# Optimization experiments

Hardware: AMD Instinct MI355X
Metric: run time of the kernel (lower is better)

The kernel has to match this reference:

```python
import jax, jax.numpy as jnp
import numpy as np

B, H, S, Dh = 4, 16, 2048, 64
NEG = -1.0e9


def setup_inputs() -> dict:
    key = jax.random.key(0)
    kq, kk, kv = jax.random.split(key, 3)
    q = jax.random.normal(kq, (B, H, S, Dh), dtype=jnp.float32)
    k = jax.random.normal(kk, (B, H, S, Dh), dtype=jnp.float32)
    v = jax.random.normal(kv, (B, H, S, Dh), dtype=jnp.float32)
    # causal mask: 1.0 where attention is disallowed (j > i), matching mask * -1e9
    mask = jnp.triu(jnp.ones((S, S), dtype=jnp.float32), k=1)[None, None, :, :]
    return {"q": q, "k": k, "v": v, "mask": mask}


def reference(q, k, v, mask):
    # scaled dot-product attention: softmax(QK^T / sqrt(Dh) + mask * -1e9) V
    dim_k = jnp.asarray(k.shape[-1], dtype=jnp.float32)
    logits = jnp.einsum("bhsd,bhtd->bhst", q, k) / jnp.sqrt(dim_k)
    logits = logits + mask * NEG
    weights = jax.nn.softmax(logits, axis=-1)
    return jnp.einsum("bhst,bhtd->bhsd", weights, v)
```

## Files before the change

kernel.cpp:

```cpp
#include <hip/hip_runtime.h>

#define S_LEN 2048
#define DH 64

typedef float f32x4 __attribute__((ext_vector_type(4)));
typedef __bf16 bf16x8 __attribute__((ext_vector_type(8)));

#define PT_STRIDE 36

__device__ __forceinline__ unsigned short f2bf(float f) {
    unsigned u = __builtin_bit_cast(unsigned, f);
    u += 0x7fffu + ((u >> 16) & 1u);
    return (unsigned short)(u >> 16);
}

__device__ __forceinline__ uint4 pack8(const float* s) {
    unsigned short h[8];
#pragma unroll
    for (int i = 0; i < 8; ++i) h[i] = f2bf(s[i]);
    return *(const uint4*)h;
}

__device__ __forceinline__ unsigned pack_rn(float a, float b) {
    unsigned ua = __builtin_bit_cast(unsigned, a) + 0x8000u;
    unsigned ub = __builtin_bit_cast(unsigned, b) + 0x8000u;
    return __builtin_amdgcn_perm(ub, ua, 0x07060302u);
}

__global__ __launch_bounds__(256) void prep_kv(const float* __restrict__ k,
                                               const float* __restrict__ v,
                                               uint4* __restrict__ kimg,
                                               uint4* __restrict__ vimg) {
    __shared__ unsigned short tr[64 * 40];
    const int bid = blockIdx.x;
    const int t = threadIdx.x;
    if (bid < 4096) {
        const int r = t >> 3, b = t & 7;
        const int srcblk = b ^ (r & 7);
        const float* src = k + ((size_t)bid * 32 + r) * 64 + srcblk * 8;
        float buf[8];
        *(float4*)&buf[0] = *(const float4*)src;
        *(float4*)&buf[4] = *(const float4*)(src + 4);
        kimg[(size_t)bid * 256 + t] = pack8(buf);
    } else {
        const int vb = bid - 4096;
        const int r = t >> 3, cb = t & 7;
        const float* src = v + ((size_t)vb * 32 + r) * 64 + cb * 8;
        float buf[8];
        *(float4*)&buf[0] = *(const float4*)src;
        *(float4*)&buf[4] = *(const float4*)(src + 4);
#pragma unroll
        for (int i = 0; i < 8; ++i)
            tr[(cb * 8 + i) * 40 + r] = f2bf(buf[i]);
        __syncthreads();
        const int d = t >> 2, kb = t & 3;
        const int skb = kb ^ ((d >> 1) & 3);
        vimg[(size_t)vb * 256 + t] = *(const uint4*)&tr[d * 40 + skb * 8];
    }
}

template <bool MASKED>
__device__ __forceinline__ void tile_body(
    const unsigned short* __restrict__ kt, const unsigned short* __restrict__ vt,
    unsigned short* __restrict__ pw,
    bf16x8 qf0, bf16x8 qf1, f32x4* acc, float& l_part,
    int jt, int ig, int quad, int c)
{
    f32x4 st[2];
    const int sw = c & 7;
#pragma unroll
    for (int mt = 0; mt < 2; ++mt) {
        const unsigned short* kr = kt + (mt * 16 + c) * 64;
        bf16x8 ka0 = __builtin_bit_cast(bf16x8, *(const uint4*)(kr + ((quad ^ sw) << 3)));
        bf16x8 ka1 = __builtin_bit_cast(bf16x8, *(const uint4*)(kr + (((quad | 4) ^ sw) << 3)));
        f32x4 a = (f32x4){0.f, 0.f, 0.f, 0.f};
        a = __builtin_amdgcn_mfma_f32_16x16x32_bf16(ka0, qf0, a, 0, 0, 0);
        a = __builtin_amdgcn_mfma_f32_16x16x32_bf16(ka1, qf1, a, 0, 0, 0);
        st[mt] = a;
    }

    float p[8];
#pragma unroll
    for (int mt = 0; mt < 2; ++mt)
#pragma unroll
        for (int r = 0; r < 4; ++r) {
            float e = exp2f(st[mt][r]);
            if (MASKED) {
                const int jg = jt * 32 + mt * 16 + quad * 4 + r;
                e = (jg > ig) ? 0.f : e;
            }
            p[mt * 4 + r] = e;
        }
    const float s01 = (p[0] + p[1]) + (p[2] + p[3]);
    const float s23 = (p[4] + p[5]) + (p[6] + p[7]);
    l_part += s01 + s23;

    unsigned* pb = (unsigned*)pw + c * (PT_STRIDE / 2);
#pragma unroll
    for (int mt = 0; mt < 2; ++mt)
#pragma unroll
        for (int rp = 0; rp < 2; ++rp)
            pb[mt * 8 + quad * 2 + rp] = pack_rn(p[mt * 4 + 2 * rp], p[mt * 4 + 2 * rp + 1]);

    const unsigned short* pr = pw + c * PT_STRIDE + quad * 8;
    uint2 lo = *(const uint2*)pr;
    uint2 hi = *(const uint2*)(pr + 4);
    uint4 pu; pu.x = lo.x; pu.y = lo.y; pu.z = hi.x; pu.w = hi.y;
    bf16x8 pf = __builtin_bit_cast(bf16x8, pu);

    const int vsw = (c >> 1) & 3;
#pragma unroll
    for (int dc = 0; dc < 4; ++dc) {
        const unsigned short* vp = vt + (dc * 16 + c) * 32 + ((quad ^ vsw) << 3);
        bf16x8 vf = __builtin_bit_cast(bf16x8, *(const uint4*)vp);
        acc[dc] = __builtin_amdgcn_mfma_f32_16x16x32_bf16(pf, vf, acc[dc], 0, 0, 0);
    }
}

__global__ __launch_bounds__(256) void fa_kernel(
    const float* __restrict__ q,
    const uint4* __restrict__ kimg,
    const uint4* __restrict__ vimg,
    float* __restrict__ out)
{
    __shared__ unsigned short kt[32 * 64];
    __shared__ unsigned short vt[64 * 32];
    __shared__ unsigned short pt[4][16 * PT_STRIDE];

    const int tid  = threadIdx.x;
    const int lane = tid & 63;
    const int wave = tid >> 6;
    const int quad = lane >> 4;
    const int c    = lane & 15;

    const int bid  = blockIdx.x;
    const int bh   = bid & 63;
    const int qblk = 31 - (bid >> 6);

    const int qtile   = qblk * 4 + wave;
    const int qbase   = qtile * 16;
    const int diag    = qtile >> 1;
    const int jt_last = 2 * qblk + 1;

    const size_t head_off = (size_t)bh * S_LEN * DH;

    const float SCALE = 0.125f * 1.4426950408889634f;
    const float* qrow = q + head_off + (size_t)(qbase + c) * DH;
    float qtmp[8];
#pragma unroll
    for (int i = 0; i < 8; ++i) qtmp[i] = qrow[quad * 8 + i] * SCALE;
    bf16x8 qf0 = __builtin_bit_cast(bf16x8, pack8(qtmp));
#pragma unroll
    for (int i = 0; i < 8; ++i) qtmp[i] = qrow[32 + quad * 8 + i] * SCALE;
    bf16x8 qf1 = __builtin_bit_cast(bf16x8, pack8(qtmp));

    f32x4 acc[4];
#pragma unroll
    for (int dc = 0; dc < 4; ++dc) acc[dc] = (f32x4){0.f, 0.f, 0.f, 0.f};
    float l_part = 0.f;
    const int ig = qbase + c;

    const uint4* kin = kimg + (size_t)bh * 64 * 256 + tid;
    const uint4* vin = vimg + (size_t)bh * 64 * 256 + tid;
    unsigned short* pw = pt[wave];

    uint4 kreg = kin[0];
    uint4 vreg = vin[0];
    for (int jt = 0; jt <= jt_last; ++jt) {
        __syncthreads();
        ((uint4*)kt)[tid] = kreg;
        ((uint4*)vt)[tid] = vreg;
        if (jt < jt_last) {
            kreg = kin[(jt + 1) * 256];
            vreg = vin[(jt + 1) * 256];
        }
        __syncthreads();

        if (jt < diag)
            tile_body<false>(kt, vt, pw, qf0, qf1, acc, l_part, jt, ig, quad, c);
        else if (jt == diag)
            tile_body<true>(kt, vt, pw, qf0, qf1, acc, l_part, jt, ig, quad, c);
    }

    float l_full = l_part;
    l_full += __shfl_xor(l_full, 16, 64);
    l_full += __shfl_xor(l_full, 32, 64);
    const float inv = 1.0f / l_full;
    float linv[4];
#pragma unroll
    for (int r = 0; r < 4; ++r)
        linv[r] = __shfl(inv, (quad << 4) + quad * 4 + r, 64);

    float* ob = out + head_off;
#pragma unroll
    for (int dc = 0; dc < 4; ++dc)
#pragma unroll
        for (int r = 0; r < 4; ++r) {
            const size_t idx = (size_t)(qbase + quad * 4 + r) * DH + dc * 16 + c;
            ob[idx] = acc[dc][r] * linv[r];
        }
}

#define KT_STRIDE 88
#define VT_STRIDE 36
__global__ __launch_bounds__(256) void fa_kernel_fb(
    const float* __restrict__ q, const float* __restrict__ k,
    const float* __restrict__ v, float* __restrict__ out)
{
    __shared__ unsigned short kt[32 * KT_STRIDE];
    __shared__ unsigned short vt[64 * VT_STRIDE];
    __shared__ unsigned short pt[4][16 * 40];
    const int tid = threadIdx.x, lane = tid & 63, wave = tid >> 6;
    const int quad = lane >> 4, c = lane & 15;
    const int bid = blockIdx.x, bh = bid & 63, qblk = 31 - (bid >> 6);
    const int qtile = qblk * 4 + wave, qbase = qtile * 16;
    const int my_diag = qtile >> 1, jt_last = (qblk * 4 + 3) >> 1;
    const size_t head_off = (size_t)bh * S_LEN * DH;
    const float* qrow = q + head_off + (size_t)(qbase + c) * DH;
    float qtmp[8];
#pragma unroll
    for (int i = 0; i < 8; ++i) qtmp[i] = qrow[quad * 8 + i];
    bf16x8 qf0 = __builtin_bit_cast(bf16x8, pack8(qtmp));
#pragma unroll
    for (int i = 0; i < 8; ++i) qtmp[i] = qrow[32 + quad * 8 + i];
    bf16x8 qf1 = __builtin_bit_cast(bf16x8, pack8(qtmp));
    f32x4 acc[4];
#pragma unroll
    for (int dc = 0; dc < 4; ++dc) acc[dc] = (f32x4){0.f, 0.f, 0.f, 0.f};
    float m_run = -1e30f, l_run = 0.f;
    const int ig = qbase + c;
    const int srow = tid >> 3, sdb = tid & 7;
    const int vcol = (((srow >> 3) ^ (sdb & 3)) << 3) | (srow & 7);
    const float LOG2E = 1.4426950408889634f;
    for (int jt = 0; jt <= jt_last; ++jt) {
        __syncthreads();
        {
            const size_t g = head_off + (size_t)(jt * 32 + srow) * DH + sdb * 8;
            float kbuf[8];
            *(float4*)&kbuf[0] = *(const float4*)(k + g);
            *(float4*)&kbuf[4] = *(const float4*)(k + g + 4);
            *(uint4*)&kt[srow * KT_STRIDE + sdb * 8] = pack8(kbuf);
            float vbuf[8];
            *(float4*)&vbuf[0] = *(const float4*)(v + g);
            *(float4*)&vbuf[4] = *(const float4*)(v + g + 4);
#pragma unroll
            for (int i = 0; i < 8; ++i)
                vt[(sdb * 8 + i) * VT_STRIDE + vcol] = f2bf(vbuf[i]);
        }
        __syncthreads();
        if (jt > my_diag) continue;
        f32x4 st[2];
#pragma unroll
        for (int mt = 0; mt < 2; ++mt) {
            const unsigned short* krow = &kt[(mt * 16 + c) * KT_STRIDE + quad * 8];
            bf16x8 ka0 = __builtin_bit_cast(bf16x8, *(const uint4*)krow);
            bf16x8 ka1 = __builtin_bit_cast(bf16x8, *(const uint4*)(krow + 32));
            f32x4 a = (f32x4){0.f, 0.f, 0.f, 0.f};
            a = __builtin_amdgcn_mfma_f32_16x16x32_bf16(ka0, qf0, a, 0, 0, 0);
            a = __builtin_amdgcn_mfma_f32_16x16x32_bf16(ka1, qf1, a, 0, 0, 0);
            st[mt] = a;
        }
        float tv[8];
#pragma unroll
        for (int mt = 0; mt < 2; ++mt)
#pragma unroll
            for (int r = 0; r < 4; ++r) {
                const int jg = jt * 32 + mt * 16 + quad * 4 + r;
                const float s = st[mt][r] * 0.125f;
                tv[mt * 4 + r] = (jg > ig) ? -1e30f : s;
            }
        float tm = tv[0];
#pragma unroll
        for (int i = 1; i < 8; ++i) tm = fmaxf(tm, tv[i]);
        tm = fmaxf(tm, __shfl_xor(tm, 16, 64));
        tm = fmaxf(tm, __shfl_xor(tm, 32, 64));
        const float m_new = fmaxf(m_run, tm);
        const float mb = m_new * LOG2E;
        float p[8], ps = 0.f;
#pragma unroll
        for (int i = 0; i < 8; ++i) { p[i] = exp2f(tv[i] * LOG2E - mb); ps += p[i]; }
        ps += __shfl_xor(ps, 16, 64);
        ps += __shfl_xor(ps, 32, 64);
        const float alpha = exp2f((m_run - m_new) * LOG2E);
        l_run = l_run * alpha + ps;
        m_run = m_new;
        unsigned short* pwf = pt[wave];
#pragma unroll
        for (int mt = 0; mt < 2; ++mt)
#pragma unroll
            for (int r = 0; r < 4; ++r)
                pwf[c * 40 + mt * 16 + quad * 4 + r] = f2bf(p[mt * 4 + r]);
        float ar[4];
#pragma unroll
        for (int r = 0; r < 4; ++r)
            ar[r] = __shfl(alpha, (quad << 4) + quad * 4 + r, 64);
#pragma unroll
        for (int dc = 0; dc < 4; ++dc)
#pragma unroll
            for (int r = 0; r < 4; ++r) acc[dc][r] *= ar[r];
        bf16x8 pf = __builtin_bit_cast(bf16x8, *(const uint4*)&pwf[c * 40 + quad * 8]);
#pragma unroll
        for (int dc = 0; dc < 4; ++dc) {
            const int vrow = dc * 16 + c;
            const int blk = quad ^ ((vrow >> 3) & 3);
            const unsigned short* vp = &vt[vrow * VT_STRIDE + blk * 8];
            uint2 a0 = *(const uint2*)vp;
            uint2 a1 = *(const uint2*)(vp + 4);
            uint4 u; u.x = a0.x; u.y = a0.y; u.z = a1.x; u.w = a1.y;
            bf16x8 vf = __builtin_bit_cast(bf16x8, u);
            acc[dc] = __builtin_amdgcn_mfma_f32_16x16x32_bf16(pf, vf, acc[dc], 0, 0, 0);
        }
    }
    float linv[4];
#pragma unroll
    for (int r = 0; r < 4; ++r) {
        const float lr = __shfl(l_run, (quad << 4) + quad * 4 + r, 64);
        linv[r] = 1.0f / lr;
    }
    float* ob = out + head_off;
#pragma unroll
    for (int dc = 0; dc < 4; ++dc)
#pragma unroll
        for (int r = 0; r < 4; ++r) {
            const size_t idx = (size_t)(qbase + quad * 4 + r) * DH + dc * 16 + c;
            ob[idx] = acc[dc][r] * linv[r];
        }
}

extern "C" void kernel_launch(void* const* d_in, const int* in_sizes, int n_in,
                              void* d_out, int out_size, void* d_ws, size_t ws_size,
                              hipStream_t stream) {
    const float* q = (const float*)d_in[0];
    const float* k = (const float*)d_in[1];
    const float* v = (const float*)d_in[2];
    float* o = (float*)d_out;
    const size_t need = (size_t)2 * 64 * 64 * 4096;
    if (ws_size >= need) {
        uint4* kimg = (uint4*)d_ws;
        uint4* vimg = kimg + (size_t)64 * 64 * 256;
        hipLaunchKernelGGL(prep_kv, dim3(8192), dim3(256), 0, stream, k, v, kimg, vimg);
        hipLaunchKernelGGL(fa_kernel, dim3(2048), dim3(256), 0, stream, q, kimg, vimg, o);
    } else {
        hipLaunchKernelGGL(fa_kernel_fb, dim3(2048), dim3(256), 0, stream, q, k, v, o);
    }
}
```

Before: 203.8 us.

## Process 32 query rows per wave with 64-key tiles and MFMA row sums

```diff
diff --git a/kernel.cpp b/kernel.cpp
--- a/kernel.cpp
+++ b/kernel.cpp
@@ -6,7 +6,7 @@
 typedef float f32x4 __attribute__((ext_vector_type(4)));
 typedef __bf16 bf16x8 __attribute__((ext_vector_type(8)));
 
-#define PT_STRIDE 36
+#define PTS 72
 
 __device__ __forceinline__ unsigned short f2bf(float f) {
     unsigned u = __builtin_bit_cast(unsigned, f);
@@ -21,10 +21,13 @@
     return *(const uint4*)h;
 }
 
-__device__ __forceinline__ unsigned pack_rn(float a, float b) {
-    unsigned ua = __builtin_bit_cast(unsigned, a) + 0x8000u;
-    unsigned ub = __builtin_bit_cast(unsigned, b) + 0x8000u;
-    return __builtin_amdgcn_perm(ub, ua, 0x07060302u);
+__device__ __forceinline__ unsigned pack_tr(float a, float b) {
+    return __builtin_amdgcn_perm(__builtin_bit_cast(unsigned, b),
+                                 __builtin_bit_cast(unsigned, a), 0x07060302u);
+}
+
+__device__ __forceinline__ bf16x8 ld128(const unsigned short* p) {
+    return __builtin_bit_cast(bf16x8, *(const uint4*)p);
 }
 
 __global__ __launch_bounds__(256) void prep_kv(const float* __restrict__ k,
@@ -59,73 +62,89 @@
     }
 }
 
-template <bool MASKED>
-__device__ __forceinline__ void tile_body(
+template <int DIAG>
+__device__ __forceinline__ void body64(
     const unsigned short* __restrict__ kt, const unsigned short* __restrict__ vt,
-    unsigned short* __restrict__ pw,
-    bf16x8 qf0, bf16x8 qf1, f32x4* acc, float& l_part,
-    int jt, int ig, int quad, int c)
+    unsigned short* __restrict__ pw0, unsigned short* __restrict__ pw1,
+    const bf16x8* qf, f32x4 acc[2][4], f32x4* accl,
+    int jt, int qbase, int quad, int c)
 {
-    f32x4 st[2];
     const int sw = c & 7;
-#pragma unroll
-    for (int mt = 0; mt < 2; ++mt) {
+    const unsigned ones_u = 0x3F803F80u;
+    uint4 ou; ou.x = ones_u; ou.y = ones_u; ou.z = ones_u; ou.w = ones_u;
+    const bf16x8 ones = __builtin_bit_cast(bf16x8, ou);
+    const int MTN = (DIAG == 1) ? 2 : 4;
+
+#pragma unroll
+    for (int mt = 0; mt < MTN; ++mt) {
         const unsigned short* kr = kt + (mt * 16 + c) * 64;
-        bf16x8 ka0 = __builtin_bit_cast(bf16x8, *(const uint4*)(kr + ((quad ^ sw) << 3)));
-        bf16x8 ka1 = __builtin_bit_cast(bf16x8, *(const uint4*)(kr + (((quad | 4) ^ sw) << 3)));
-        f32x4 a = (f32x4){0.f, 0.f, 0.f, 0.f};
-        a = __builtin_amdgcn_mfma_f32_16x16x32_bf16(ka0, qf0, a, 0, 0, 0);
-        a = __builtin_amdgcn_mfma_f32_16x16x32_bf16(ka1, qf1, a, 0, 0, 0);
-        st[mt] = a;
-    }
-
-    float p[8];
-#pragma unroll
-    for (int mt = 0; mt < 2; ++mt)
-#pragma unroll
-        for (int r = 0; r < 4; ++r) {
-            float e = exp2f(st[mt][r]);
-            if (MASKED) {
-                const int jg = jt * 32 + mt * 16 + quad * 4 + r;
-                e = (jg > ig) ? 0.f : e;
+        bf16x8 ka0 = ld128(kr + ((quad ^ sw) << 3));
+        bf16x8 ka1 = ld128(kr + (((quad | 4) ^ sw) << 3));
+        f32x4 s0 = (f32x4){0.f, 0.f, 0.f, 0.f};
+        f32x4 s1 = (f32x4){0.f, 0.f, 0.f, 0.f};
+        s0 = __builtin_amdgcn_mfma_f32_16x16x32_bf16(ka0, qf[0], s0, 0, 0, 0);
+        s0 = __builtin_amdgcn_mfma_f32_16x16x32_bf16(ka1, qf[1], s0, 0, 0, 0);
+        s1 = __builtin_amdgcn_mfma_f32_16x16x32_bf16(ka0, qf[2], s1, 0, 0, 0);
+        s1 = __builtin_amdgcn_mfma_f32_16x16x32_bf16(ka1, qf[3], s1, 0, 0, 0);
+
+        const bool MASKMT = (DIAG == 1) || (DIAG == 2 && mt >= 2);
+#pragma unroll
+        for (int s = 0; s < 2; ++s) {
+            const f32x4 st = s ? s1 : s0;
+            const int ig = qbase + s * 16 + c;
+            float p[4];
+#pragma unroll
+            for (int r = 0; r < 4; ++r) {
+                float e = exp2f(st[r]);
+                if (MASKMT) {
+                    const int jg = jt * 64 + mt * 16 + quad * 4 + r;
+                    e = (jg > ig) ? 0.f : e;
+                }
+                p[r] = e;
             }
-            p[mt * 4 + r] = e;
-        }
-    const float s01 = (p[0] + p[1]) + (p[2] + p[3]);
-    const float s23 = (p[4] + p[5]) + (p[6] + p[7]);
-    l_part += s01 + s23;
-
-    unsigned* pb = (unsigned*)pw + c * (PT_STRIDE / 2);
-#pragma unroll
-    for (int mt = 0; mt < 2; ++mt)
-#pragma unroll
-        for (int rp = 0; rp < 2; ++rp)
-            pb[mt * 8 + quad * 2 + rp] = pack_rn(p[mt * 4 + 2 * rp], p[mt * 4 + 2 * rp + 1]);
-
-    const unsigned short* pr = pw + c * PT_STRIDE + quad * 8;
-    uint2 lo = *(const uint2*)pr;
-    uint2 hi = *(const uint2*)(pr + 4);
-    uint4 pu; pu.x = lo.x; pu.y = lo.y; pu.z = hi.x; pu.w = hi.y;
-    bf16x8 pf = __builtin_bit_cast(bf16x8, pu);
+            unsigned a = pack_tr(p[0], p[1]);
+            unsigned b = pack_tr(p[2], p[3]);
+            unsigned* pb = (unsigned*)(s ? pw1 : pw0) + c * (PTS / 2) + mt * 8 + quad * 2;
+            *(uint2*)pb = make_uint2(a, b);
+        }
+    }
+
+    bf16x8 pf00 = ld128(pw0 + c * PTS + quad * 8);
+    bf16x8 pf10 = ld128(pw1 + c * PTS + quad * 8);
+    accl[0] = __builtin_amdgcn_mfma_f32_16x16x32_bf16(pf00, ones, accl[0], 0, 0, 0);
+    accl[1] = __builtin_amdgcn_mfma_f32_16x16x32_bf16(pf10, ones, accl[1], 0, 0, 0);
+    bf16x8 pf01, pf11;
+    if (DIAG != 1) {
+        pf01 = ld128(pw0 + c * PTS + 32 + quad * 8);
+        pf11 = ld128(pw1 + c * PTS + 32 + quad * 8);
+        accl[0] = __builtin_amdgcn_mfma_f32_16x16x32_bf16(pf01, ones, accl[0], 0, 0, 0);
+        accl[1] = __builtin_amdgcn_mfma_f32_16x16x32_bf16(pf11, ones, accl[1], 0, 0, 0);
+    }
 
     const int vsw = (c >> 1) & 3;
 #pragma unroll
     for (int dc = 0; dc < 4; ++dc) {
-        const unsigned short* vp = vt + (dc * 16 + c) * 32 + ((quad ^ vsw) << 3);
-        bf16x8 vf = __builtin_bit_cast(bf16x8, *(const uint4*)vp);
-        acc[dc] = __builtin_amdgcn_mfma_f32_16x16x32_bf16(pf, vf, acc[dc], 0, 0, 0);
-    }
-}
-
-__global__ __launch_bounds__(256) void fa_kernel(
+        const unsigned short* vr = vt + (dc * 16 + c) * 32 + ((quad ^ vsw) << 3);
+        bf16x8 vf0 = ld128(vr);
+        acc[0][dc] = __builtin_amdgcn_mfma_f32_16x16x32_bf16(pf00, vf0, acc[0][dc], 0, 0, 0);
+        acc[1][dc] = __builtin_amdgcn_mfma_f32_16x16x32_bf16(pf10, vf0, acc[1][dc], 0, 0, 0);
+        if (DIAG != 1) {
+            bf16x8 vf1 = ld128(vr + 2048);
+            acc[0][dc] = __builtin_amdgcn_mfma_f32_16x16x32_bf16(pf01, vf1, acc[0][dc], 0, 0, 0);
+            acc[1][dc] = __builtin_amdgcn_mfma_f32_16x16x32_bf16(pf11, vf1, acc[1][dc], 0, 0, 0);
+        }
+    }
+}
+
+__global__ __launch_bounds__(256, 4) void fa_kernel(
     const float* __restrict__ q,
     const uint4* __restrict__ kimg,
     const uint4* __restrict__ vimg,
     float* __restrict__ out)
 {
-    __shared__ unsigned short kt[32 * 64];
-    __shared__ unsigned short vt[64 * 32];
-    __shared__ unsigned short pt[4][16 * PT_STRIDE];
+    __shared__ unsigned short kt[64 * 64];
+    __shared__ unsigned short vt[2 * 64 * 32];
+    __shared__ unsigned short pt[4][2][16 * PTS];
 
     const int tid  = threadIdx.x;
     const int lane = tid & 63;
@@ -135,70 +154,80 @@
 
     const int bid  = blockIdx.x;
     const int bh   = bid & 63;
-    const int qblk = 31 - (bid >> 6);
-
-    const int qtile   = qblk * 4 + wave;
-    const int qbase   = qtile * 16;
-    const int diag    = qtile >> 1;
+    const int qblk = bid >> 6;
+
+    const int wt      = qblk * 4 + wave;
+    const int qbase   = wt * 32;
+    const int my_diag = wt >> 1;
     const int jt_last = 2 * qblk + 1;
 
     const size_t head_off = (size_t)bh * S_LEN * DH;
 
     const float SCALE = 0.125f * 1.4426950408889634f;
-    const float* qrow = q + head_off + (size_t)(qbase + c) * DH;
-    float qtmp[8];
-#pragma unroll
-    for (int i = 0; i < 8; ++i) qtmp[i] = qrow[quad * 8 + i] * SCALE;
-    bf16x8 qf0 = __builtin_bit_cast(bf16x8, pack8(qtmp));
-#pragma unroll
-    for (int i = 0; i < 8; ++i) qtmp[i] = qrow[32 + quad * 8 + i] * SCALE;
-    bf16x8 qf1 = __builtin_bit_cast(bf16x8, pack8(qtmp));
-
-    f32x4 acc[4];
-#pragma unroll
-    for (int dc = 0; dc < 4; ++dc) acc[dc] = (f32x4){0.f, 0.f, 0.f, 0.f};
-    float l_part = 0.f;
-    const int ig = qbase + c;
+    bf16x8 qf[4];
+#pragma unroll
+    for (int s = 0; s < 2; ++s) {
+        const float* qrow = q + head_off + (size_t)(qbase + s * 16 + c) * DH;
+        float t0[8], t1[8];
+#pragma unroll
+        for (int i = 0; i < 8; ++i) t0[i] = qrow[quad * 8 + i] * SCALE;
+#pragma unroll
+        for (int i = 0; i < 8; ++i) t1[i] = qrow[32 + quad * 8 + i] * SCALE;
+        qf[s * 2 + 0] = __builtin_bit_cast(bf16x8, pack8(t0));
+        qf[s * 2 + 1] = __builtin_bit_cast(bf16x8, pack8(t1));
+    }
+
+    f32x4 acc[2][4];
+#pragma unroll
+    for (int s = 0; s < 2; ++s)
+#pragma unroll
+        for (int dc = 0; dc < 4; ++dc) acc[s][dc] = (f32x4){0.f, 0.f, 0.f, 0.f};
+    f32x4 accl[2];
+    accl[0] = (f32x4){0.f, 0.f, 0.f, 0.f};
+    accl[1] = (f32x4){0.f, 0.f, 0.f, 0.f};
 
     const uint4* kin = kimg + (size_t)bh * 64 * 256 + tid;
     const uint4* vin = vimg + (size_t)bh * 64 * 256 + tid;
-    unsigned short* pw = pt[wave];
-
-    uint4 kreg = kin[0];
-    uint4 vreg = vin[0];
+    unsigned short* pw0 = pt[wave][0];
+    unsigned short* pw1 = pt[wave][1];
+
+    uint4 kA = kin[0], kB = kin[256];
+    uint4 vA = vin[0], vB = vin[256];
     for (int jt = 0; jt <= jt_last; ++jt) {
         __syncthreads();
-        ((uint4*)kt)[tid] = kreg;
-        ((uint4*)vt)[tid] = vreg;
+        ((uint4*)kt)[tid] = kA;  ((uint4*)kt)[tid + 256] = kB;
+        ((uint4*)vt)[tid] = vA;  ((uint4*)vt)[tid + 256] = vB;
         if (jt < jt_last) {
-            kreg = kin[(jt + 1) * 256];
-            vreg = vin[(jt + 1) * 256];
-        }
-        __syncthreads();
-
-        if (jt < diag)
-            tile_body<false>(kt, vt, pw, qf0, qf1, acc, l_part, jt, ig, quad, c);
-        else if (jt == diag)
-            tile_body<true>(kt, vt, pw, qf0, qf1, acc, l_part, jt, ig, quad, c);
-    }
-
-    float l_full = l_part;
-    l_full += __shfl_xor(l_full, 16, 64);
-    l_full += __shfl_xor(l_full, 32, 64);
-    const float inv = 1.0f / l_full;
-    float linv[4];
-#pragma unroll
-    for (int r = 0; r < 4; ++r)
-        linv[r] = __shfl(inv, (quad << 4) + quad * 4 + r, 64);
+            kA = kin[(jt + 1) * 512];  kB = kin[(jt + 1) * 512 + 256];
+            vA = vin[(jt + 1) * 512];  vB = vin[(jt + 1) * 512 + 256];
+        }
+        __syncthreads();
+
+        if (jt < my_diag) {
+            body64<0>(kt, vt, pw0, pw1, qf, acc, accl, jt, qbase, quad, c);
+        } else if (jt == my_diag) {
+            if ((wt & 1) == 0)
+                body64<1>(kt, vt, pw0, pw1, qf, acc, accl, jt, qbase, quad, c);
+            else
+                body64<2>(kt, vt, pw0, pw1, qf, acc, accl, jt, qbase, quad, c);
+        }
+    }
 
     float* ob = out + head_off;
 #pragma unroll
-    for (int dc = 0; dc < 4; ++dc)
-#pragma unroll
-        for (int r = 0; r < 4; ++r) {
-            const size_t idx = (size_t)(qbase + quad * 4 + r) * DH + dc * 16 + c;
-            ob[idx] = acc[dc][r] * linv[r];
-        }
+    for (int s = 0; s < 2; ++s) {
+        float linv[4];
+#pragma unroll
+        for (int r = 0; r < 4; ++r) linv[r] = 1.0f / accl[s][r];
+#pragma unroll
+        for (int dc = 0; dc < 4; ++dc)
+#pragma unroll
+            for (int r = 0; r < 4; ++r) {
+                const size_t idx =
+                    (size_t)(qbase + s * 16 + quad * 4 + r) * DH + dc * 16 + c;
+                ob[idx] = acc[s][dc][r] * linv[r];
+            }
+    }
 }
 
 #define KT_STRIDE 88
@@ -207,9 +236,9 @@
     const float* __restrict__ q, const float* __restrict__ k,
     const float* __restrict__ v, float* __restrict__ out)
 {
-    __shared__ unsigned short kt[32 * KT_STRIDE];
-    __shared__ unsigned short vt[64 * VT_STRIDE];
-    __shared__ unsigned short pt[4][16 * 40];
+    __shared__ unsigned short kts[32 * KT_STRIDE];
+    __shared__ unsigned short vts[64 * VT_STRIDE];
+    __shared__ unsigned short pts[4][16 * 40];
     const int tid = threadIdx.x, lane = tid & 63, wave = tid >> 6;
     const int quad = lane >> 4, c = lane & 15;
     const int bid = blockIdx.x, bh = bid & 63, qblk = 31 - (bid >> 6);
@@ -239,20 +268,20 @@
             float kbuf[8];
             *(float4*)&kbuf[0] = *(const float4*)(k + g);
             *(float4*)&kbuf[4] = *(const float4*)(k + g + 4);
-            *(uint4*)&kt[srow * KT_STRIDE + sdb * 8] = pack8(kbuf);
+            *(uint4*)&kts[srow * KT_STRIDE + sdb * 8] = pack8(kbuf);
             float vbuf[8];
             *(float4*)&vbuf[0] = *(const float4*)(v + g);
             *(float4*)&vbuf[4] = *(const float4*)(v + g + 4);
 #pragma unroll
             for (int i = 0; i < 8; ++i)
-                vt[(sdb * 8 + i) * VT_STRIDE + vcol] = f2bf(vbuf[i]);
+                vts[(sdb * 8 + i) * VT_STRIDE + vcol] = f2bf(vbuf[i]);
         }
         __syncthreads();
         if (jt > my_diag) continue;
         f32x4 st[2];
 #pragma unroll
         for (int mt = 0; mt < 2; ++mt) {
-            const unsigned short* krow = &kt[(mt * 16 + c) * KT_STRIDE + quad * 8];
+            const unsigned short* krow = &kts[(mt * 16 + c) * KT_STRIDE + quad * 8];
             bf16x8 ka0 = __builtin_bit_cast(bf16x8, *(const uint4*)krow);
             bf16x8 ka1 = __builtin_bit_cast(bf16x8, *(const uint4*)(krow + 32));
             f32x4 a = (f32x4){0.f, 0.f, 0.f, 0.f};
@@ -284,7 +313,7 @@
         const float alpha = exp2f((m_run - m_new) * LOG2E);
         l_run = l_run * alpha + ps;
         m_run = m_new;
-        unsigned short* pwf = pt[wave];
+        unsigned short* pwf = pts[wave];
 #pragma unroll
         for (int mt = 0; mt < 2; ++mt)
 #pragma unroll
@@ -303,7 +332,7 @@
         for (int dc = 0; dc < 4; ++dc) {
             const int vrow = dc * 16 + c;
             const int blk = quad ^ ((vrow >> 3) & 3);
-            const unsigned short* vp = &vt[vrow * VT_STRIDE + blk * 8];
+            const unsigned short* vp = &vts[vrow * VT_STRIDE + blk * 8];
             uint2 a0 = *(const uint2*)vp;
             uint2 a1 = *(const uint2*)(vp + 4);
             uint4 u; u.x = a0.x; u.y = a0.y; u.z = a1.x; u.w = a1.y;
@@ -339,7 +368,7 @@
         uint4* kimg = (uint4*)d_ws;
         uint4* vimg = kimg + (size_t)64 * 64 * 256;
         hipLaunchKernelGGL(prep_kv, dim3(8192), dim3(256), 0, stream, k, v, kimg, vimg);
-        hipLaunchKernelGGL(fa_kernel, dim3(2048), dim3(256), 0, stream, q, kimg, vimg, o);
+        hipLaunchKernelGGL(fa_kernel, dim3(1024), dim3(256), 0, stream, q, kimg, vimg, o);
     } else {
         hipLaunchKernelGGL(fa_kernel_fb, dim3(2048), dim3(256), 0, stream, q, k, v, o);
     }
```

Measured after the change: 209.0 us. 2.5% more time.

## Compute softmax row sums via MFMA with ones vector, use raw exp2 and truncating pack

Applied to the files above, without the earlier changes.

```diff
diff --git a/kernel.cpp b/kernel.cpp
--- a/kernel.cpp
+++ b/kernel.cpp
@@ -7,6 +7,7 @@
 typedef __bf16 bf16x8 __attribute__((ext_vector_type(8)));
 
 #define PT_STRIDE 36
+#define MFMA16(A, B, C) __builtin_amdgcn_mfma_f32_16x16x32_bf16(A, B, C, 0, 0, 0)
 
 __device__ __forceinline__ unsigned short f2bf(float f) {
     unsigned u = __builtin_bit_cast(unsigned, f);
@@ -21,10 +22,18 @@
     return *(const uint4*)h;
 }
 
-__device__ __forceinline__ unsigned pack_rn(float a, float b) {
-    unsigned ua = __builtin_bit_cast(unsigned, a) + 0x8000u;
-    unsigned ub = __builtin_bit_cast(unsigned, b) + 0x8000u;
-    return __builtin_amdgcn_perm(ub, ua, 0x07060302u);
+__device__ __forceinline__ unsigned pack_tr(float a, float b) {
+    return __builtin_amdgcn_perm(__builtin_bit_cast(unsigned, b),
+                                 __builtin_bit_cast(unsigned, a), 0x07060302u);
+}
+
+__device__ __forceinline__ bf16x8 ld128(const unsigned short* p) {
+    return __builtin_bit_cast(bf16x8, *(const uint4*)p);
+}
+
+__device__ __forceinline__ bf16x8 ones8() {
+    uint4 ou; ou.x = 0x3F803F80u; ou.y = ou.x; ou.z = ou.x; ou.w = ou.x;
+    return __builtin_bit_cast(bf16x8, ou);
 }
 
 __global__ __launch_bounds__(256) void prep_kv(const float* __restrict__ k,
@@ -63,7 +72,7 @@
 __device__ __forceinline__ void tile_body(
     const unsigned short* __restrict__ kt, const unsigned short* __restrict__ vt,
     unsigned short* __restrict__ pw,
-    bf16x8 qf0, bf16x8 qf1, f32x4* acc, float& l_part,
+    bf16x8 qf0, bf16x8 qf1, f32x4* acc, f32x4& accl,
     int jt, int ig, int quad, int c)
 {
     f32x4 st[2];
@@ -71,11 +80,11 @@
 #pragma unroll
     for (int mt = 0; mt < 2; ++mt) {
         const unsigned short* kr = kt + (mt * 16 + c) * 64;
-        bf16x8 ka0 = __builtin_bit_cast(bf16x8, *(const uint4*)(kr + ((quad ^ sw) << 3)));
-        bf16x8 ka1 = __builtin_bit_cast(bf16x8, *(const uint4*)(kr + (((quad | 4) ^ sw) << 3)));
+        bf16x8 ka0 = ld128(kr + ((quad ^ sw) << 3));
+        bf16x8 ka1 = ld128(kr + (((quad | 4) ^ sw) << 3));
         f32x4 a = (f32x4){0.f, 0.f, 0.f, 0.f};
-        a = __builtin_amdgcn_mfma_f32_16x16x32_bf16(ka0, qf0, a, 0, 0, 0);
-        a = __builtin_amdgcn_mfma_f32_16x16x32_bf16(ka1, qf1, a, 0, 0, 0);
+        a = MFMA16(ka0, qf0, a);
+        a = MFMA16(ka1, qf1, a);
         st[mt] = a;
     }
 
@@ -84,23 +93,22 @@
     for (int mt = 0; mt < 2; ++mt)
 #pragma unroll
         for (int r = 0; r < 4; ++r) {
-            float e = exp2f(st[mt][r]);
+            float e = __builtin_amdgcn_exp2f(st[mt][r]);
             if (MASKED) {
                 const int jg = jt * 32 + mt * 16 + quad * 4 + r;
                 e = (jg > ig) ? 0.f : e;
             }
             p[mt * 4 + r] = e;
         }
-    const float s01 = (p[0] + p[1]) + (p[2] + p[3]);
-    const float s23 = (p[4] + p[5]) + (p[6] + p[7]);
-    l_part += s01 + s23;
 
     unsigned* pb = (unsigned*)pw + c * (PT_STRIDE / 2);
 #pragma unroll
-    for (int mt = 0; mt < 2; ++mt)
-#pragma unroll
-        for (int rp = 0; rp < 2; ++rp)
-            pb[mt * 8 + quad * 2 + rp] = pack_rn(p[mt * 4 + 2 * rp], p[mt * 4 + 2 * rp + 1]);
+    for (int mt = 0; mt < 2; ++mt) {
+        uint2 w;
+        w.x = pack_tr(p[mt * 4 + 0], p[mt * 4 + 1]);
+        w.y = pack_tr(p[mt * 4 + 2], p[mt * 4 + 3]);
+        *(uint2*)(pb + mt * 8 + quad * 2) = w;
+    }
 
     const unsigned short* pr = pw + c * PT_STRIDE + quad * 8;
     uint2 lo = *(const uint2*)pr;
@@ -108,12 +116,13 @@
     uint4 pu; pu.x = lo.x; pu.y = lo.y; pu.z = hi.x; pu.w = hi.y;
     bf16x8 pf = __builtin_bit_cast(bf16x8, pu);
 
+    accl = MFMA16(pf, ones8(), accl);
+
     const int vsw = (c >> 1) & 3;
 #pragma unroll
     for (int dc = 0; dc < 4; ++dc) {
         const unsigned short* vp = vt + (dc * 16 + c) * 32 + ((quad ^ vsw) << 3);
-        bf16x8 vf = __builtin_bit_cast(bf16x8, *(const uint4*)vp);
-        acc[dc] = __builtin_amdgcn_mfma_f32_16x16x32_bf16(pf, vf, acc[dc], 0, 0, 0);
+        acc[dc] = MFMA16(pf, ld128(vp), acc[dc]);
     }
 }
 
@@ -157,7 +166,7 @@
     f32x4 acc[4];
 #pragma unroll
     for (int dc = 0; dc < 4; ++dc) acc[dc] = (f32x4){0.f, 0.f, 0.f, 0.f};
-    float l_part = 0.f;
+    f32x4 accl = (f32x4){0.f, 0.f, 0.f, 0.f};
     const int ig = qbase + c;
 
     const uint4* kin = kimg + (size_t)bh * 64 * 256 + tid;
@@ -177,19 +186,14 @@
         __syncthreads();
 
         if (jt < diag)
-            tile_body<false>(kt, vt, pw, qf0, qf1, acc, l_part, jt, ig, quad, c);
+            tile_body<false>(kt, vt, pw, qf0, qf1, acc, accl, jt, ig, quad, c);
         else if (jt == diag)
-            tile_body<true>(kt, vt, pw, qf0, qf1, acc, l_part, jt, ig, quad, c);
-    }
-
-    float l_full = l_part;
-    l_full += __shfl_xor(l_full, 16, 64);
-    l_full += __shfl_xor(l_full, 32, 64);
-    const float inv = 1.0f / l_full;
+            tile_body<true>(kt, vt, pw, qf0, qf1, acc, accl, jt, ig, quad, c);
+    }
+
     float linv[4];
 #pragma unroll
-    for (int r = 0; r < 4; ++r)
-        linv[r] = __shfl(inv, (quad << 4) + quad * 4 + r, 64);
+    for (int r = 0; r < 4; ++r) linv[r] = 1.0f / accl[r];
 
     float* ob = out + head_off;
 #pragma unroll
@@ -207,9 +211,9 @@
     const float* __restrict__ q, const float* __restrict__ k,
     const float* __restrict__ v, float* __restrict__ out)
 {
-    __shared__ unsigned short kt[32 * KT_STRIDE];
-    __shared__ unsigned short vt[64 * VT_STRIDE];
-    __shared__ unsigned short pt[4][16 * 40];
+    __shared__ unsigned short kts[32 * KT_STRIDE];
+    __shared__ unsigned short vts[64 * VT_STRIDE];
+    __shared__ unsigned short pts[4][16 * 40];
     const int tid = threadIdx.x, lane = tid & 63, wave = tid >> 6;
     const int quad = lane >> 4, c = lane & 15;
     const int bid = blockIdx.x, bh = bid & 63, qblk = 31 - (bid >> 6);
@@ -239,25 +243,25 @@
             float kbuf[8];
             *(float4*)&kbuf[0] = *(const float4*)(k + g);
             *(float4*)&kbuf[4] = *(const float4*)(k + g + 4);
-            *(uint4*)&kt[srow * KT_STRIDE + sdb * 8] = pack8(kbuf);
+            *(uint4*)&kts[srow * KT_STRIDE + sdb * 8] = pack8(kbuf);
             float vbuf[8];
             *(float4*)&vbuf[0] = *(const float4*)(v + g);
             *(float4*)&vbuf[4] = *(const float4*)(v + g + 4);
 #pragma unroll
             for (int i = 0; i < 8; ++i)
-                vt[(sdb * 8 + i) * VT_STRIDE + vcol] = f2bf(vbuf[i]);
+                vts[(sdb * 8 + i) * VT_STRIDE + vcol] = f2bf(vbuf[i]);
         }
         __syncthreads();
         if (jt > my_diag) continue;
         f32x4 st[2];
 #pragma unroll
         for (int mt = 0; mt < 2; ++mt) {
-            const unsigned short* krow = &kt[(mt * 16 + c) * KT_STRIDE + quad * 8];
+            const unsigned short* krow = &kts[(mt * 16 + c) * KT_STRIDE + quad * 8];
             bf16x8 ka0 = __builtin_bit_cast(bf16x8, *(const uint4*)krow);
             bf16x8 ka1 = __builtin_bit_cast(bf16x8, *(const uint4*)(krow + 32));
             f32x4 a = (f32x4){0.f, 0.f, 0.f, 0.f};
-            a = __builtin_amdgcn_mfma_f32_16x16x32_bf16(ka0, qf0, a, 0, 0, 0);
-            a = __builtin_amdgcn_mfma_f32_16x16x32_bf16(ka1, qf1, a, 0, 0, 0);
+            a = MFMA16(ka0, qf0, a);
+            a = MFMA16(ka1, qf1, a);
             st[mt] = a;
         }
         float tv[8];
@@ -278,13 +282,16 @@
         const float mb = m_new * LOG2E;
         float p[8], ps = 0.f;
 #pragma unroll
-        for (int i = 0; i < 8; ++i) { p[i] = exp2f(tv[i] * LOG2E - mb); ps += p[i]; }
+        for (int i = 0; i < 8; ++i) {
+            p[i] = __builtin_amdgcn_exp2f(tv[i] * LOG2E - mb);
+            ps += p[i];
+        }
         ps += __shfl_xor(ps, 16, 64);
         ps += __shfl_xor(ps, 32, 64);
-        const float alpha = exp2f((m_run - m_new) * LOG2E);
+        const float alpha = __builtin_amdgcn_exp2f((m_run - m_new) * LOG2E);
         l_run = l_run * alpha + ps;
         m_run = m_new;
-        unsigned short* pwf = pt[wave];
+        unsigned short* pwf = pts[wave];
 #pragma unroll
         for (int mt = 0; mt < 2; ++mt)
 #pragma unroll
@@ -303,12 +310,12 @@
         for (int dc = 0; dc < 4; ++dc) {
             const int vrow = dc * 16 + c;
             const int blk = quad ^ ((vrow >> 3) & 3);
-            const unsigned short* vp = &vt[vrow * VT_STRIDE + blk * 8];
+            const unsigned short* vp = &vts[vrow * VT_STRIDE + blk * 8];
             uint2 a0 = *(const uint2*)vp;
             uint2 a1 = *(const uint2*)(vp + 4);
             uint4 u; u.x = a0.x; u.y = a0.y; u.z = a1.x; u.w = a1.y;
             bf16x8 vf = __builtin_bit_cast(bf16x8, u);
-            acc[dc] = __builtin_amdgcn_mfma_f32_16x16x32_bf16(pf, vf, acc[dc], 0, 0, 0);
+            acc[dc] = MFMA16(pf, vf, acc[dc]);
         }
     }
     float linv[4];
```

Result: faster. 194.3 us (-4.7%).
